# Kernel optimization log

Measured on AMD Instinct MI355X. Metric: run time of the kernel, lower is better.

Reference implementation:

```python
import jax, jax.numpy as jnp
import numpy as np

N_NODES = 100000
N_EDGES = 1600000
IN_DIM = 128
OUT_DIM = 128


def setup_inputs() -> dict:
    key = jax.random.key(0)
    k1, k2, k3, k4, k5 = jax.random.split(key, 5)
    h = jax.random.normal(k1, (N_NODES, IN_DIM), dtype=jnp.float32)
    # nn.Linear(in_dim, out_dim): W [out, in], b [out]
    W = jax.random.normal(k2, (OUT_DIM, IN_DIM), dtype=jnp.float32) * (1.0 / np.sqrt(IN_DIM))
    b = jax.random.normal(k3, (OUT_DIM,), dtype=jnp.float32) * 0.01
    edge_src = jax.random.randint(k4, (N_EDGES,), 0, N_NODES, dtype=jnp.int32)
    edge_dst = jax.random.randint(k5, (N_EDGES,), 0, N_NODES, dtype=jnp.int32)
    return {"h": h, "W": W, "b": b, "edge_src": edge_src, "edge_dst": edge_dst}


def reference(h, W, b, edge_src, edge_dst):
    n = h.shape[0]
    # in-degree of each node (edges point src -> dst), clamped to >= 1
    deg = jax.ops.segment_sum(jnp.ones_like(edge_dst, dtype=h.dtype), edge_dst, num_segments=n)
    norm = jnp.power(jnp.clip(deg, 1.0), -0.5)[:, None]  # [N, 1]
    hn = h * norm
    # copy_u + sum: gather source features, scatter-add to destinations (SpMM)
    agg = jax.ops.segment_sum(hn[edge_src], edge_dst, num_segments=n)  # [N, in_dim]
    out = (agg * norm) @ W.T + b
    return out
```

## Files before the change

### kernel.cpp

```cpp
#include <hip/hip_runtime.h>
#include <hip/hip_fp16.h>

#define DIM 128
#define TSH 8
#define TSZ 256
#define QSZ 64
#define EBLK 4096
#define TCAP 5120
#define CAPQ 1280

typedef _Float16 half8_t __attribute__((ext_vector_type(8)));
typedef float f32x4 __attribute__((ext_vector_type(4)));
typedef float f32x4v __attribute__((ext_vector_type(4)));


__global__ __launch_bounds__(1024) void kA_scatter(const int* __restrict__ src,
                                                   const int* __restrict__ dst,
                                                   int* __restrict__ cursor,
                                                   unsigned* __restrict__ tbuf,
                                                   int ne, int neb, int nt,
                                                   const float* __restrict__ W,
                                                   _Float16* __restrict__ Wf) {
    __shared__ int hist[512];
    __shared__ int sst[512];
    __shared__ int cur[512];
    __shared__ int gbase[512];
    __shared__ int ps[256];
    __shared__ unsigned sval[EBLK];
    __shared__ unsigned short skey[EBLK];
    int t = threadIdx.x, blk = blockIdx.x;
    if (blk >= neb) {
        int ii = blk - neb;
        if (ii < 2) {
            int idx = ii * 1024 + t;
            int ct = idx >> 8, kk = (idx >> 6) & 3, lane = idx & 63;
            int nn = lane & 15, quad = lane >> 4;
            const float* wr = W + (ct * 16 + nn) * DIM + kk * 32 + quad * 8;
            _Float16* o = Wf + (size_t)idx * 8;
#pragma unroll
            for (int j = 0; j < 8; ++j) o[j] = (_Float16)wr[j];
        }
        return;
    }
    if (t < 512) hist[t] = 0;
    __syncthreads();
    int e0 = blk * EBLK;
    int e1 = e0 + EBLK; if (e1 > ne) e1 = ne;
    for (int i = e0 + t; i < e1; i += 1024)
        atomicAdd(&hist[dst[i] >> TSH], 1);
    __syncthreads();
    int h0 = 0, h1 = 0;
    if (t < 256) { h0 = hist[2 * t]; h1 = hist[2 * t + 1]; ps[t] = h0 + h1; }
    __syncthreads();
    for (int off = 1; off < 256; off <<= 1) {
        int v = (t < 256 && t >= off) ? ps[t - off] : 0;
        __syncthreads();
        if (t < 256) ps[t] += v;
        __syncthreads();
    }
    if (t < 256) {
        int ex0 = ps[t] - h0 - h1;
        sst[2 * t] = ex0;     sst[2 * t + 1] = ex0 + h0;
        cur[2 * t] = ex0;     cur[2 * t + 1] = ex0 + h0;
    }
    __syncthreads();
    if (t < 512) {
        int c = hist[t];
        gbase[t] = (c > 0) ? atomicAdd(&cursor[t], c) : 0;
    }
    __syncthreads();
    for (int i = e0 + t; i < e1; i += 1024) {
        int d = dst[i];
        int key = d >> TSH;
        int r = atomicAdd(&cur[key], 1);
        sval[r] = ((unsigned)src[i] << TSH) | (unsigned)(d & (TSZ - 1));
        skey[r] = (unsigned short)key;
    }
    __syncthreads();
    int cnt = e1 - e0;
    for (int p = t; p < cnt; p += 1024) {
        int k = skey[p];
        int o = gbase[k] + (p - sst[k]);
        if (o < TCAP) tbuf[(size_t)k * TCAP + o] = sval[p];
    }
}

__global__ __launch_bounds__(1024) void kB_deg_hn(const unsigned* __restrict__ tbuf,
                                                  const int* __restrict__ cursor,
                                                  const float* __restrict__ hsrc,
                                                  float2* __restrict__ hn, int n) {
    __shared__ int hist[TSZ];
    __shared__ float scl[TSZ];
    int t = threadIdx.x, tile = blockIdx.x;
    if (t < 256) hist[t] = 0;
    __syncthreads();
    int cnt = cursor[tile]; if (cnt > TCAP) cnt = TCAP;
    int ts = tile * TCAP, te = ts + cnt;
    for (int i = ts + t; i < te; i += 1024)
        atomicAdd(&hist[tbuf[i] & (TSZ - 1)], 1);
    __syncthreads();
    if (t < 256) {
        int d = hist[t];
        scl[t] = rsqrtf((float)(d > 1 ? d : 1));
    }
    __syncthreads();
    int qbase = tile * 8192;
    for (int q = t; q < 8192; q += 1024) {
        int node = tile * TSZ + (q >> 5);
        if (node < n) {
            f32x4v v = __builtin_nontemporal_load((const f32x4v*)hsrc + qbase + q);
            float sc = scl[q >> 5];
            union { __half2 h2[2]; float2 f2; } u;
            u.h2[0] = __floats2half2_rn(v.x * sc, v.y * sc);
            u.h2[1] = __floats2half2_rn(v.z * sc, v.w * sc);
            hn[qbase + q] = u.f2;
        }
    }
}

__global__ __launch_bounds__(512) void kC_tile_gemm(
        const unsigned* __restrict__ tbuf, const int* __restrict__ cursor,
        const float2* __restrict__ hn, const _Float16* __restrict__ Wf,
        const float* __restrict__ b, float* __restrict__ out,
        int n, int nt) {
    __shared__ int hist[QSZ];
    __shared__ int sst[QSZ];
    __shared__ int cur[QSZ];
    __shared__ float scl[QSZ];
    __shared__ int cntq;
    __shared__ unsigned elB[CAPQ];
    __shared__ _Float16 xs[64 * 136];
    int t = threadIdx.x;
    int c = blockIdx.x & 7, j = blockIdx.x >> 3;
    int tile = c + 8 * (j >> 2), q = j & 3;
    if (tile >= nt) return;

    int cnt = cursor[tile]; if (cnt > TCAP) cnt = TCAP;
    int ts = tile * TCAP, te = ts + cnt;
    if (t < QSZ) hist[t] = 0;
    __syncthreads();
    for (int i = ts + t; i < te; i += 512) {
        unsigned p = tbuf[i];
        int dl = (int)(p & (TSZ - 1));
        if ((dl >> 6) == q) atomicAdd(&hist[dl & (QSZ - 1)], 1);
    }
    __syncthreads();
    if (t < QSZ) {
        int d = hist[t];
        int x = d;
#pragma unroll
        for (int off = 1; off < 64; off <<= 1) {
            int y = __shfl_up(x, off, 64);
            if (t >= off) x += y;
        }
        sst[t] = x - d;
        cur[t] = x - d;
        scl[t] = rsqrtf((float)(d > 1 ? d : 1));
        if (t == QSZ - 1) cntq = x;
    }
    __syncthreads();
    bool fast = (cntq <= CAPQ);
    if (fast) {
        for (int i = ts + t; i < te; i += 512) {
            unsigned p = tbuf[i];
            int dl = (int)(p & (TSZ - 1));
            if ((dl >> 6) == q) {
                int r = atomicAdd(&cur[dl & (QSZ - 1)], 1);
                elB[r] = p >> TSH;
            }
        }
        __syncthreads();
    }

    int g2 = t >> 5, lane2 = t & 31;
#pragma unroll
    for (int it = 0; it < 4; ++it) {
        int row = it * 16 + g2;
        union { __half2 h2[2]; float2 f2; } u;
        __half2 a0 = __floats2half2_rn(0.f, 0.f), a1 = a0;
        if (fast) {
            int s0 = sst[row];
            int jend = s0 + hist[row];
            int jj = s0;
            for (; jj + 7 < jend; jj += 8) {
                int e0 = elB[jj], e1 = elB[jj + 1], e2 = elB[jj + 2], e3 = elB[jj + 3];
                int e4 = elB[jj + 4], e5 = elB[jj + 5], e6 = elB[jj + 6], e7 = elB[jj + 7];
                float2 r0 = hn[(size_t)e0 * 32 + lane2];
                float2 r1 = hn[(size_t)e1 * 32 + lane2];
                float2 r2 = hn[(size_t)e2 * 32 + lane2];
                float2 r3 = hn[(size_t)e3 * 32 + lane2];
                float2 r4 = hn[(size_t)e4 * 32 + lane2];
                float2 r5 = hn[(size_t)e5 * 32 + lane2];
                float2 r6 = hn[(size_t)e6 * 32 + lane2];
                float2 r7 = hn[(size_t)e7 * 32 + lane2];
                const __half2* q0 = (const __half2*)&r0;
                const __half2* q1 = (const __half2*)&r1;
                const __half2* q2 = (const __half2*)&r2;
                const __half2* q3 = (const __half2*)&r3;
                const __half2* q4 = (const __half2*)&r4;
                const __half2* q5 = (const __half2*)&r5;
                const __half2* q6 = (const __half2*)&r6;
                const __half2* q7 = (const __half2*)&r7;
                a0 = __hadd2(a0, q0[0]); a1 = __hadd2(a1, q0[1]);
                a0 = __hadd2(a0, q1[0]); a1 = __hadd2(a1, q1[1]);
                a0 = __hadd2(a0, q2[0]); a1 = __hadd2(a1, q2[1]);
                a0 = __hadd2(a0, q3[0]); a1 = __hadd2(a1, q3[1]);
                a0 = __hadd2(a0, q4[0]); a1 = __hadd2(a1, q4[1]);
                a0 = __hadd2(a0, q5[0]); a1 = __hadd2(a1, q5[1]);
                a0 = __hadd2(a0, q6[0]); a1 = __hadd2(a1, q6[1]);
                a0 = __hadd2(a0, q7[0]); a1 = __hadd2(a1, q7[1]);
            }
            for (; jj + 3 < jend; jj += 4) {
                int e0 = elB[jj], e1 = elB[jj + 1], e2 = elB[jj + 2], e3 = elB[jj + 3];
                float2 r0 = hn[(size_t)e0 * 32 + lane2];
                float2 r1 = hn[(size_t)e1 * 32 + lane2];
                float2 r2 = hn[(size_t)e2 * 32 + lane2];
                float2 r3 = hn[(size_t)e3 * 32 + lane2];
                const __half2* q0 = (const __half2*)&r0;
                const __half2* q1 = (const __half2*)&r1;
                const __half2* q2 = (const __half2*)&r2;
                const __half2* q3 = (const __half2*)&r3;
                a0 = __hadd2(a0, q0[0]); a1 = __hadd2(a1, q0[1]);
                a0 = __hadd2(a0, q1[0]); a1 = __hadd2(a1, q1[1]);
                a0 = __hadd2(a0, q2[0]); a1 = __hadd2(a1, q2[1]);
                a0 = __hadd2(a0, q3[0]); a1 = __hadd2(a1, q3[1]);
            }
            for (; jj < jend; ++jj) {
                float2 r0 = hn[(size_t)elB[jj] * 32 + lane2];
                const __half2* q0 = (const __half2*)&r0;
                a0 = __hadd2(a0, q0[0]); a1 = __hadd2(a1, q0[1]);
            }
        } else {
            int want = (q << 6) | row;
            for (int i = ts; i < te; ++i) {
                unsigned p = tbuf[i];
                if ((int)(p & (TSZ - 1)) == want) {
                    float2 r0 = hn[(size_t)(p >> TSH) * 32 + lane2];
                    const __half2* q0 = (const __half2*)&r0;
                    a0 = __hadd2(a0, q0[0]); a1 = __hadd2(a1, q0[1]);
                }
            }
        }
        float nd = scl[row];
        float2 f0 = __half22float2(a0), f1 = __half22float2(a1);
        u.h2[0] = __floats2half2_rn(f0.x * nd, f0.y * nd);
        u.h2[1] = __floats2half2_rn(f1.x * nd, f1.y * nd);
        *(float2*)(xs + row * 136 + lane2 * 4) = u.f2;
    }
    __syncthreads();

    int w = t >> 6, wl = t & 63, cn = wl & 15, quad = wl >> 4;
    f32x4 acc4[4] = {{0.f, 0.f, 0.f, 0.f}, {0.f, 0.f, 0.f, 0.f},
                     {0.f, 0.f, 0.f, 0.f}, {0.f, 0.f, 0.f, 0.f}};
#pragma unroll
    for (int kk = 0; kk < 4; ++kk) {
        half8_t bf = ((const half8_t*)Wf)[(w * 4 + kk) * 64 + wl];
#pragma unroll
        for (int rt = 0; rt < 4; ++rt) {
            half8_t af = *(const half8_t*)(xs + (rt * 16 + cn) * 136 + kk * 32 + quad * 8);
            acc4[rt] = __builtin_amdgcn_mfma_f32_16x16x32_f16(af, bf, acc4[rt], 0, 0, 0);
        }
    }
    float bj = b[w * 16 + cn];
    int node0 = tile * TSZ + q * QSZ;
#pragma unroll
    for (int rt = 0; rt < 4; ++rt) {
#pragma unroll
        for (int r = 0; r < 4; ++r) {
            int node = node0 + rt * 16 + quad * 4 + r;
            if (node < n)
                __builtin_nontemporal_store(acc4[rt][r] + bj,
                                            &out[(size_t)node * DIM + w * 16 + cn]);
        }
    }
}

extern "C" void kernel_launch(void* const* d_in, const int* in_sizes, int n_in,
                              void* d_out, int out_size, void* d_ws, size_t ws_size,
                              hipStream_t stream) {
    const float* h = (const float*)d_in[0];
    const float* W = (const float*)d_in[1];
    const float* b = (const float*)d_in[2];
    const int* esrc = (const int*)d_in[3];
    const int* edst = (const int*)d_in[4];
    float* out = (float*)d_out;

    int n = in_sizes[0] / DIM;
    int ne = in_sizes[3];

    int neb = (ne + EBLK - 1) / EBLK;
    int nt = (n + TSZ - 1) >> TSH;

    float2* hn = (float2*)d_ws;
    _Float16* Wf = (_Float16*)(hn + (size_t)n * 32);
    int* cursor = (int*)(Wf + 16384);
    unsigned* tbuf = (unsigned*)(cursor + 512);

    hipMemsetAsync(cursor, 0, 512 * sizeof(int), stream);
    kA_scatter<<<neb + 2, 1024, 0, stream>>>(esrc, edst, cursor, tbuf,
                                             ne, neb, nt, W, Wf);
    kB_deg_hn<<<nt, 1024, 0, stream>>>(tbuf, cursor, h, hn, n);
    int P = ((nt + 7) / 8) * 4;
    kC_tile_gemm<<<8 * P, 512, 0, stream>>>(tbuf, cursor, hn, Wf, b, out, n, nt);
}
```

Measured before the change: 203.2 us.

## Stage edges in LDS once and split degree/normalize kernel for wider parallelism

The scatter kernel now reads src/dst once into a staging LDS buffer during the histogram pass, instead of re-reading global memory in the binning pass. The combined degree-and-normalize kernel, which ran only ~391 blocks of 1024 threads, is split in two. One small kernel writes per-node norm values to workspace, and a grid-stride kernel with 2048 blocks converts h to scaled fp16. This aims to raise memory parallelism on the bandwidth-bound h conversion, at the cost of an extra launch, a norm array round-trip, and doubled LDS use in the scatter kernel.

```diff
diff --git a/kernel.cpp b/kernel.cpp
--- a/kernel.cpp
+++ b/kernel.cpp
@@ -26,8 +26,10 @@
     __shared__ int cur[512];
     __shared__ int gbase[512];
     __shared__ int ps[256];
-    __shared__ unsigned sval[EBLK];
-    __shared__ unsigned short skey[EBLK];
+    __shared__ unsigned sval_r[EBLK];
+    __shared__ unsigned short skey_r[EBLK];
+    __shared__ unsigned sval_s[EBLK];
+    __shared__ unsigned short skey_s[EBLK];
     int t = threadIdx.x, blk = blockIdx.x;
     if (blk >= neb) {
         int ii = blk - neb;
@@ -46,8 +48,16 @@
     __syncthreads();
     int e0 = blk * EBLK;
     int e1 = e0 + EBLK; if (e1 > ne) e1 = ne;
-    for (int i = e0 + t; i < e1; i += 1024)
-        atomicAdd(&hist[dst[i] >> TSH], 1);
+    int cnt = e1 - e0;
+    for (int i = e0 + t; i < e1; i += 1024) {
+        int d = dst[i];
+        int s = src[i];
+        int key = d >> TSH;
+        int p = i - e0;
+        sval_r[p] = ((unsigned)s << TSH) | (unsigned)(d & (TSZ - 1));
+        skey_r[p] = (unsigned short)key;
+        atomicAdd(&hist[key], 1);
+    }
     __syncthreads();
     int h0 = 0, h1 = 0;
     if (t < 256) { h0 = hist[2 * t]; h1 = hist[2 * t + 1]; ps[t] = h0 + h1; }
@@ -69,52 +79,50 @@
         gbase[t] = (c > 0) ? atomicAdd(&cursor[t], c) : 0;
     }
     __syncthreads();
-    for (int i = e0 + t; i < e1; i += 1024) {
-        int d = dst[i];
-        int key = d >> TSH;
-        int r = atomicAdd(&cur[key], 1);
-        sval[r] = ((unsigned)src[i] << TSH) | (unsigned)(d & (TSZ - 1));
-        skey[r] = (unsigned short)key;
-    }
-    __syncthreads();
-    int cnt = e1 - e0;
     for (int p = t; p < cnt; p += 1024) {
-        int k = skey[p];
+        int k = skey_r[p];
+        int r = atomicAdd(&cur[k], 1);
+        sval_s[r] = sval_r[p];
+        skey_s[r] = (unsigned short)k;
+    }
+    __syncthreads();
+    for (int p = t; p < cnt; p += 1024) {
+        int k = skey_s[p];
         int o = gbase[k] + (p - sst[k]);
-        if (o < TCAP) tbuf[(size_t)k * TCAP + o] = sval[p];
-    }
-}
-
-__global__ __launch_bounds__(1024) void kB_deg_hn(const unsigned* __restrict__ tbuf,
-                                                  const int* __restrict__ cursor,
-                                                  const float* __restrict__ hsrc,
-                                                  float2* __restrict__ hn, int n) {
+        if (o < TCAP) tbuf[(size_t)k * TCAP + o] = sval_s[p];
+    }
+}
+
+__global__ __launch_bounds__(256) void kB1_norm(const unsigned* __restrict__ tbuf,
+                                                const int* __restrict__ cursor,
+                                                float* __restrict__ norm, int n) {
     __shared__ int hist[TSZ];
-    __shared__ float scl[TSZ];
     int t = threadIdx.x, tile = blockIdx.x;
-    if (t < 256) hist[t] = 0;
+    hist[t] = 0;
     __syncthreads();
     int cnt = cursor[tile]; if (cnt > TCAP) cnt = TCAP;
     int ts = tile * TCAP, te = ts + cnt;
-    for (int i = ts + t; i < te; i += 1024)
+    for (int i = ts + t; i < te; i += 256)
         atomicAdd(&hist[tbuf[i] & (TSZ - 1)], 1);
     __syncthreads();
-    if (t < 256) {
+    int node = tile * TSZ + t;
+    if (node < n) {
         int d = hist[t];
-        scl[t] = rsqrtf((float)(d > 1 ? d : 1));
-    }
-    __syncthreads();
-    int qbase = tile * 8192;
-    for (int q = t; q < 8192; q += 1024) {
-        int node = tile * TSZ + (q >> 5);
-        if (node < n) {
-            f32x4v v = __builtin_nontemporal_load((const f32x4v*)hsrc + qbase + q);
-            float sc = scl[q >> 5];
-            union { __half2 h2[2]; float2 f2; } u;
-            u.h2[0] = __floats2half2_rn(v.x * sc, v.y * sc);
-            u.h2[1] = __floats2half2_rn(v.z * sc, v.w * sc);
-            hn[qbase + q] = u.f2;
-        }
+        norm[node] = rsqrtf((float)(d > 1 ? d : 1));
+    }
+}
+
+__global__ __launch_bounds__(256) void kB2_hn(const float* __restrict__ hsrc,
+                                              const float* __restrict__ norm,
+                                              float2* __restrict__ hn, int n32) {
+    int stride = gridDim.x * 256;
+    for (int i = blockIdx.x * 256 + threadIdx.x; i < n32; i += stride) {
+        float sc = norm[i >> 5];
+        f32x4v v = __builtin_nontemporal_load((const f32x4v*)hsrc + i);
+        union { __half2 h2[2]; float2 f2; } u;
+        u.h2[0] = __floats2half2_rn(v.x * sc, v.y * sc);
+        u.h2[1] = __floats2half2_rn(v.z * sc, v.w * sc);
+        hn[i] = u.f2;
     }
 }
 
@@ -287,6 +295,7 @@
 
     int n = in_sizes[0] / DIM;
     int ne = in_sizes[3];
+    int n32 = n * 32;
 
     int neb = (ne + EBLK - 1) / EBLK;
     int nt = (n + TSZ - 1) >> TSH;
@@ -294,12 +303,14 @@
     float2* hn = (float2*)d_ws;
     _Float16* Wf = (_Float16*)(hn + (size_t)n * 32);
     int* cursor = (int*)(Wf + 16384);
-    unsigned* tbuf = (unsigned*)(cursor + 512);
+    float* norm = (float*)(cursor + 512);
+    unsigned* tbuf = (unsigned*)(norm + ((n + 3) & ~3));
 
     hipMemsetAsync(cursor, 0, 512 * sizeof(int), stream);
     kA_scatter<<<neb + 2, 1024, 0, stream>>>(esrc, edst, cursor, tbuf,
                                              ne, neb, nt, W, Wf);
-    kB_deg_hn<<<nt, 1024, 0, stream>>>(tbuf, cursor, h, hn, n);
+    kB1_norm<<<nt, 256, 0, stream>>>(tbuf, cursor, norm, n);
+    kB2_hn<<<2048, 256, 0, stream>>>(h, norm, hn, n32);
     int P = ((nt + 7) / 8) * 4;
     kC_tile_gemm<<<8 * P, 512, 0, stream>>>(tbuf, cursor, hn, Wf, b, out, n, nt);
 }
```

Measured after the change: 204.2 us. Within noise of the previous version (+0.5%).
